# Kernel optimization log

Hardware: AMD Instinct MI355X
Metric: run time of the kernel (lower is better)

## Reference

```python
import jax, jax.numpy as jnp
import numpy as np
import math

N_HEAD = 16
ROPE_BASE = 10000.0

def _rope_cos_sin(seq_len, head_dim, dtype):
    inv_freq = 1.0 / (ROPE_BASE ** (jnp.arange(0, head_dim, 2, dtype=jnp.float32) / head_dim))
    t = jnp.arange(seq_len, dtype=jnp.float32)
    freqs = t[:, None] * inv_freq[None, :]            # [S, D/2]
    emb = jnp.concatenate([freqs, freqs], axis=-1)     # [S, D]
    # broadcast shape [1, 1, S, D] to match q/k [B, H, S, D]
    return jnp.cos(emb)[None, None].astype(dtype), jnp.sin(emb)[None, None].astype(dtype)

def _rotate_half(x):
    x1, x2 = jnp.split(x, 2, axis=-1)
    return jnp.concatenate([-x2, x1], axis=-1)

def setup_inputs() -> dict:
    key = jax.random.key(0)
    ks = jax.random.split(key, 5)
    B, S, E = 2, 2048, 1024
    x = jax.random.normal(ks[0], (B, S, E), dtype=jnp.float32)
    init = 1.0 / math.sqrt(E)
    Wq = jax.random.normal(ks[1], (E, E), dtype=jnp.float32) * init
    Wk = jax.random.normal(ks[2], (E, E), dtype=jnp.float32) * init
    Wv = jax.random.normal(ks[3], (E, E), dtype=jnp.float32) * init
    Wo = jax.random.normal(ks[4], (E, E), dtype=jnp.float32) * init
    # causal mask: True = masked (masked_fill with -inf)
    attn_mask = jnp.triu(jnp.ones((S, S), dtype=bool), k=1)
    return {"x": x, "Wq": Wq, "Wk": Wk, "Wv": Wv, "Wo": Wo, "attn_mask": attn_mask}

def reference(x, Wq, Wk, Wv, Wo, attn_mask):
    B, S, E = x.shape
    H = N_HEAD
    D = E // H
    # projections (torch Linear: y = x @ W.T), split heads -> [B, H, S, D]
    def proj(W):
        return jnp.einsum('bse,fe->bsf', x, W).reshape(B, S, H, D).transpose(0, 2, 1, 3)
    q, k, v = proj(Wq), proj(Wk), proj(Wv)
    cos, sin = _rope_cos_sin(S, D, x.dtype)
    q = q * cos + _rotate_half(q) * sin
    k = k * cos + _rotate_half(k) * sin
    scale = 1.0 / math.sqrt(D)
    scores = jnp.einsum('bhqd,bhkd->bhqk', q, k) * scale  # [B, H, S, S]
    scores = jnp.where(attn_mask[None, None], -jnp.inf, scores)
    attn = jax.nn.softmax(scores, axis=-1)
    out = jnp.einsum('bhqk,bhkd->bhqd', attn, v)           # [B, H, S, D]
    out = out.transpose(0, 2, 1, 3).reshape(B, S, E)
    return jnp.einsum('bse,fe->bsf', out, Wo)
```

## Files before the change

### kernel.cpp

```cpp
#include <hip/hip_runtime.h>
#include <hip/hip_bf16.h>

#define NB 2
#define NH 16
#define SEQ 2048
#define HD 64
#define EMB 1024

typedef unsigned short u16;
typedef unsigned int u32;
typedef __attribute__((ext_vector_type(8))) short bf16x8;
typedef __attribute__((ext_vector_type(4))) float f32x4;
typedef __attribute__((ext_vector_type(8))) unsigned short us8;

__device__ __forceinline__ float b2f(u16 u) {
    union { unsigned int i; float f; } v; v.i = ((unsigned int)u) << 16; return v.f;
}
__device__ __forceinline__ u16 f2b(float f) {
    union { float f; unsigned int i; } v; v.f = f;
    unsigned int x = v.i;
    return (u16)((x + 0x7FFFu + ((x >> 16) & 1u)) >> 16);
}
__device__ __forceinline__ u32 pk2(float a, float b) {
    union { __hip_bfloat162 h; u32 u; } v;
    v.h = __float22bfloat162_rn(make_float2(a, b));
    return v.u;
}

__device__ __forceinline__ void gld16(const u16* g, u16* l) {
    __builtin_amdgcn_global_load_lds((const __attribute__((address_space(1))) void*)g,
                                     (__attribute__((address_space(3))) void*)l, 16, 0, 0);
}

__global__ __launch_bounds__(256)
void detect_dtype_54571854463007(const u16* __restrict__ x, int* __restrict__ flag) {
    __shared__ int cnt;
    if (threadIdx.x == 0) cnt = 0;
    __syncthreads();
    const u16 v = x[threadIdx.x];
    const int e = (v >> 7) & 0xFF;
    if (e >= 110 && e <= 135) atomicAdd(&cnt, 1);
    __syncthreads();
    if (threadIdx.x == 0) *flag = (cnt >= 200) ? 1 : 0;
}

__device__ __forceinline__ void conv8(const void* src, u16* dst, int i, int isbf16) {
    if (isbf16) {
        *reinterpret_cast<uint4*>(dst + i) =
            *reinterpret_cast<const uint4*>((const u16*)src + i);
    } else {
        const float* s = (const float*)src + i;
        float4 a = *reinterpret_cast<const float4*>(s);
        float4 b = *reinterpret_cast<const float4*>(s + 4);
        us8 v;
        v[0] = f2b(a.x); v[1] = f2b(a.y); v[2] = f2b(a.z); v[3] = f2b(a.w);
        v[4] = f2b(b.x); v[5] = f2b(b.y); v[6] = f2b(b.z); v[7] = f2b(b.w);
        *reinterpret_cast<us8*>(dst + i) = v;
    }
}

__global__ __launch_bounds__(256)
void convert_54571854463007(const void* __restrict__ src, u16* __restrict__ dst,
                            const int* __restrict__ flagp, int n) {
    const int i = (blockIdx.x * 256 + threadIdx.x) * 8;
    if (i >= n) return;
    conv8(src, dst, i, *flagp);
}

__global__ __launch_bounds__(256)
void convertw_54571854463007(const void* __restrict__ w0, const void* __restrict__ w1,
                             const void* __restrict__ w2, const void* __restrict__ w3,
                             u16* __restrict__ dqkv, u16* __restrict__ dob,
                             const int* __restrict__ flagp) {
    const int NW = EMB * EMB;
    const int seg = blockIdx.y;
    const void* src = (seg == 0) ? w0 : (seg == 1) ? w1 : (seg == 2) ? w2 : w3;
    u16* dst = (seg < 3) ? (dqkv + (size_t)seg * NW) : dob;
    const int i = (blockIdx.x * 256 + threadIdx.x) * 8;
    conv8(src, dst, i, *flagp);
}

template<int OUT_MODE>
__global__ __launch_bounds__(256)
void gemm_mfma_54571854463007(const u16* __restrict__ A, const u16* __restrict__ Bw,
                              void* __restrict__ C, const int* __restrict__ flagp,
                              int M, int N, int K) {
    __shared__ __align__(16) u16 As[128 * 32];
    __shared__ __align__(16) u16 Bs[128 * 32];
    const int tid  = threadIdx.x;
    const int wave = tid >> 6, lane = tid & 63;
    const int quad = lane >> 4, fr = lane & 15;
    const int wr = (wave >> 1) * 64, wc = (wave & 1) * 64;
    const int m0 = blockIdx.y * 128, n0 = blockIdx.x * 128;
    const int r0 = tid >> 2;
    const int kc = (tid & 3) * 8;
    const f32x4 zz = {0.f, 0.f, 0.f, 0.f};
    f32x4 acc[4][4];
#pragma unroll
    for (int i = 0; i < 4; ++i)
#pragma unroll
        for (int j = 0; j < 4; ++j) acc[i][j] = zz;

    for (int k0 = 0; k0 < K; k0 += 32) {
        gld16(A  + (size_t)(m0 + r0) * K + k0 + kc,      &As[wave * 512]);
        gld16(A  + (size_t)(m0 + 64 + r0) * K + k0 + kc, &As[2048 + wave * 512]);
        gld16(Bw + (size_t)(n0 + r0) * K + k0 + kc,      &Bs[wave * 512]);
        gld16(Bw + (size_t)(n0 + 64 + r0) * K + k0 + kc, &Bs[2048 + wave * 512]);
        __syncthreads();
        bf16x8 af[4], bfr[4];
#pragma unroll
        for (int mi = 0; mi < 4; ++mi)
            af[mi] = *reinterpret_cast<const bf16x8*>(&As[(wr + mi * 16 + fr) * 32 + quad * 8]);
#pragma unroll
        for (int ni = 0; ni < 4; ++ni)
            bfr[ni] = *reinterpret_cast<const bf16x8*>(&Bs[(wc + ni * 16 + fr) * 32 + quad * 8]);
#pragma unroll
        for (int mi = 0; mi < 4; ++mi)
#pragma unroll
            for (int ni = 0; ni < 4; ++ni)
                acc[mi][ni] = __builtin_amdgcn_mfma_f32_16x16x32_bf16(af[mi], bfr[ni], acc[mi][ni], 0, 0, 0);
        __syncthreads();
    }

    if (OUT_MODE == 1) {
        const int t0 = n0 >> 10;
        if (t0 == 0) {
            const float SCL = 0.18033688011112042f;
#pragma unroll
            for (int mi = 0; mi < 4; ++mi)
#pragma unroll
                for (int ni = 0; ni < 4; ++ni)
#pragma unroll
                    for (int r = 0; r < 4; ++r) acc[mi][ni][r] *= SCL;
        }
        if (t0 < 2) {
            const float inv0 = __powf(10000.f, -(float)fr / 32.f);
            const float inv1 = __powf(10000.f, -(float)(fr + 16) / 32.f);
#pragma unroll
            for (int mi = 0; mi < 4; ++mi)
#pragma unroll
                for (int r = 0; r < 4; ++r) {
                    const int s = (m0 + wr + mi * 16 + quad * 4 + r) & (SEQ - 1);
#pragma unroll
                    for (int nl = 0; nl < 2; ++nl) {
                        float sn, cs;
                        __sincosf((float)s * (nl ? inv1 : inv0), &sn, &cs);
                        const float lo = acc[mi][nl][r], hi = acc[mi][nl + 2][r];
                        acc[mi][nl][r]     = lo * cs - hi * sn;
                        acc[mi][nl + 2][r] = hi * cs + lo * sn;
                    }
                }
        }
    }

    const int isbf16 = (OUT_MODE == 0) ? *flagp : 0;
    const size_t TS = (size_t)NB * NH * SEQ * HD;
#pragma unroll
    for (int mi = 0; mi < 4; ++mi)
#pragma unroll
        for (int ni = 0; ni < 4; ++ni)
#pragma unroll
            for (int r = 0; r < 4; ++r) {
                const int m = m0 + wr + mi * 16 + quad * 4 + r;
                const int n = n0 + wc + ni * 16 + fr;
                const float v = acc[mi][ni][r];
                if (OUT_MODE == 1) {
                    const int t = n >> 10, idx = n & 1023;
                    const int h = idx >> 6, d = idx & 63;
                    const int b = m >> 11, s = m & (SEQ - 1);
                    ((u16*)C)[t * TS + ((((size_t)b * NH + h) * SEQ + s) << 6) + d] = f2b(v);
                } else {
                    if (isbf16) ((u16*)C)[(size_t)m * N + n] = f2b(v);
                    else        ((float*)C)[(size_t)m * N + n] = v;
                }
            }
}

__device__ __forceinline__ void loadK_54571854463007(const u16* Kt, int fr, int quad,
                                                     bf16x8* kc) {
#pragma unroll
    for (int nt = 0; nt < 4; ++nt) {
        const u16* kp = Kt + (size_t)(nt * 16 + fr) * HD + quad * 8;
        kc[2 * nt]     = *reinterpret_cast<const bf16x8*>(kp);
        kc[2 * nt + 1] = *reinterpret_cast<const bf16x8*>(kp + 32);
    }
}

__global__ __launch_bounds__(256)
void flash_54571854463007(const u16* __restrict__ Q, const u16* __restrict__ K,
                          const u16* __restrict__ V, u16* __restrict__ AO) {
    __shared__ __align__(16) u16 Vt[2 * 4608];
    __shared__ __align__(16) u16 Ps[4608];
    const int tid  = threadIdx.x;
    const int w    = tid >> 6, lane = tid & 63;
    const int quad = lane >> 4, fr = lane & 15;
    const int lin = blockIdx.x;
    const int xcd = lin & 7;
    const int p   = lin >> 3;
    const int qt  = 31 - (p >> 2);
    const int bh  = xcd * 4 + (p & 3);
    const int h = bh & 15, b = bh >> 4;
    const size_t base = ((size_t)b * NH + h) * SEQ * HD;
    const int k2   = (tid & 31) * 2;
    const int key0 = (k2 & 3) * 16 + (k2 >> 2);
    const int d8   = ((tid >> 5) & 7) * 8;
    const int total = qt + 1;

    const bf16x8 ones = {(short)0x3F80, (short)0x3F80, (short)0x3F80, (short)0x3F80,
                         (short)0x3F80, (short)0x3F80, (short)0x3F80, (short)0x3F80};

    const u16* qp = Q + base + (size_t)(qt * 64 + w * 16 + fr) * HD + quad * 8;
    const bf16x8 aq0 = *reinterpret_cast<const bf16x8*>(qp);
    const bf16x8 aq1 = *reinterpret_cast<const bf16x8*>(qp + 32);

    bf16x8 kc[8], kn[8];
    loadK_54571854463007(K + base, fr, quad, kc);
    us8 vc0, vc1, vn0, vn1;
    {
        const u16* vs = V + base + (size_t)key0 * HD + d8;
        vc0 = *reinterpret_cast<const us8*>(vs);
        vc1 = *reinterpret_cast<const us8*>(vs + 16 * HD);
    }

    const f32x4 zz = {0.f, 0.f, 0.f, 0.f};
    f32x4 lacc = zz;
    f32x4 oacc[4];
#pragma unroll
    for (int nt = 0; nt < 4; ++nt) oacc[nt] = zz;

    for (int j = 0; j < total; ++j) {
        const int buf   = j & 1;
        const int kt    = j;
        const int vbase = buf * 4608;
#pragma unroll
        for (int jj = 0; jj < 8; ++jj) {
            const u32 pk = ((u32)(u16)vc1[jj] << 16) | (u32)(u16)vc0[jj];
            *reinterpret_cast<u32*>(&Vt[vbase + (d8 + jj) * 72 + k2]) = pk;
        }
        __syncthreads();
        if (j + 1 < total) {
            const int nkt = j + 1;
            loadK_54571854463007(K + base + (size_t)nkt * 64 * HD, fr, quad, kn);
            const u16* vs = V + base + (size_t)(nkt * 64 + key0) * HD + d8;
            vn0 = *reinterpret_cast<const us8*>(vs);
            vn1 = *reinterpret_cast<const us8*>(vs + 16 * HD);
        }
        f32x4 sa[4];
#pragma unroll
        for (int nt = 0; nt < 4; ++nt) {
            sa[nt] = __builtin_amdgcn_mfma_f32_16x16x32_bf16(aq0, kc[2 * nt], zz, 0, 0, 0);
            sa[nt] = __builtin_amdgcn_mfma_f32_16x16x32_bf16(aq1, kc[2 * nt + 1], sa[nt], 0, 0, 0);
        }
        if (kt == qt) {
#pragma unroll
            for (int nt = 0; nt < 4; ++nt)
#pragma unroll
                for (int r = 0; r < 4; ++r)
                    if (nt * 16 + fr > w * 16 + quad * 4 + r) sa[nt][r] = -__builtin_inff();
        }
#pragma unroll
        for (int r = 0; r < 4; ++r) {
            const float p0 = exp2f(sa[0][r]);
            const float p1 = exp2f(sa[1][r]);
            const float p2 = exp2f(sa[2][r]);
            const float p3 = exp2f(sa[3][r]);
            *reinterpret_cast<uint2*>(&Ps[(w * 16 + quad * 4 + r) * 72 + 4 * fr]) =
                make_uint2(pk2(p0, p1), pk2(p2, p3));
        }
        bf16x8 ap0 = *reinterpret_cast<const bf16x8*>(&Ps[(w * 16 + fr) * 72 + quad * 8]);
        bf16x8 ap1 = *reinterpret_cast<const bf16x8*>(&Ps[(w * 16 + fr) * 72 + 32 + quad * 8]);
        lacc = __builtin_amdgcn_mfma_f32_16x16x32_bf16(ap0, ones, lacc, 0, 0, 0);
        lacc = __builtin_amdgcn_mfma_f32_16x16x32_bf16(ap1, ones, lacc, 0, 0, 0);
#pragma unroll
        for (int nt = 0; nt < 4; ++nt) {
            bf16x8 bv0 = *reinterpret_cast<const bf16x8*>(&Vt[vbase + (nt * 16 + fr) * 72 + quad * 8]);
            bf16x8 bv1 = *reinterpret_cast<const bf16x8*>(&Vt[vbase + (nt * 16 + fr) * 72 + 32 + quad * 8]);
            oacc[nt] = __builtin_amdgcn_mfma_f32_16x16x32_bf16(ap0, bv0, oacc[nt], 0, 0, 0);
            oacc[nt] = __builtin_amdgcn_mfma_f32_16x16x32_bf16(ap1, bv1, oacc[nt], 0, 0, 0);
        }
#pragma unroll
        for (int i = 0; i < 8; ++i) kc[i] = kn[i];
        vc0 = vn0; vc1 = vn1;
    }
#pragma unroll
    for (int r = 0; r < 4; ++r) {
        const float inv = 1.0f / lacc[r];
        const int q = qt * 64 + w * 16 + quad * 4 + r;
#pragma unroll
        for (int nt = 0; nt < 4; ++nt)
            AO[(((size_t)b * SEQ + q) * NH + h) * HD + nt * 16 + fr] = f2b(oacc[nt][r] * inv);
    }
}

extern "C" void kernel_launch(void* const* d_in, const int* in_sizes, int n_in,
                              void* d_out, int out_size, void* d_ws, size_t ws_size,
                              hipStream_t stream) {
    (void)in_sizes; (void)n_in; (void)out_size; (void)ws_size;
    const void* x  = d_in[0];
    const void* Wq = d_in[1];
    const void* Wk = d_in[2];
    const void* Wv = d_in[3];
    const void* Wo = d_in[4];

    char* ws = (char*)d_ws;
    const size_t MB = 1024 * 1024;
    int* flag = (int*)ws;
    u16* xb   = (u16*)(ws + 64);
    u16* Wqkv = (u16*)(ws + 64 + 8 * MB);
    u16* Wob  = (u16*)(ws + 64 + 14 * MB);
    u16* Qb   = (u16*)(ws + 64 + 16 * MB);
    u16* Kb   = (u16*)(ws + 64 + 24 * MB);
    u16* Vb   = (u16*)(ws + 64 + 32 * MB);
    u16* AO   = xb;

    detect_dtype_54571854463007<<<1, 256, 0, stream>>>((const u16*)x, flag);

    const int NX = NB * SEQ * EMB;
    const int NW = EMB * EMB;
    convert_54571854463007<<<NX / 2048, 256, 0, stream>>>(x, xb, flag, NX);
    convertw_54571854463007<<<dim3(NW / 2048, 4), 256, 0, stream>>>(Wq, Wk, Wv, Wo, Wqkv, Wob, flag);

    const int M = NB * SEQ;
    gemm_mfma_54571854463007<1><<<dim3(3 * EMB / 128, M / 128), 256, 0, stream>>>(
        xb, Wqkv, Qb, flag, M, 3 * EMB, EMB);

    flash_54571854463007<<<dim3(1024), 256, 0, stream>>>(Qb, Kb, Vb, AO);

    gemm_mfma_54571854463007<0><<<dim3(EMB / 128, M / 128), 256, 0, stream>>>(
        AO, Wob, d_out, flag, M, EMB, EMB);
}
```

Before: 245.5 us.

## Stage K tiles in swizzled LDS and pass P through bpermute instead of LDS

K tiles now go through a double-buffered, XOR-swizzled LDS buffer using direct global-to-LDS loads (gld16) rather than per-lane register prefetch. The QK^T MFMA operands are swapped so scores come out transposed. This lets the softmax probabilities be redistributed across lanes with ds_bpermute instead of a round trip through the shared Ps buffer. Launch bounds request four blocks per CU to raise occupancy. The aim is to cut register pressure and LDS traffic, at the cost of more cross-lane permutes and a bigger LDS footprint for K.

Measured after the change: 214.4 us. 12.7% less time.

```diff
diff --git a/kernel.cpp b/kernel.cpp
--- a/kernel.cpp
+++ b/kernel.cpp
@@ -176,21 +176,11 @@
             }
 }
 
-__device__ __forceinline__ void loadK_54571854463007(const u16* Kt, int fr, int quad,
-                                                     bf16x8* kc) {
-#pragma unroll
-    for (int nt = 0; nt < 4; ++nt) {
-        const u16* kp = Kt + (size_t)(nt * 16 + fr) * HD + quad * 8;
-        kc[2 * nt]     = *reinterpret_cast<const bf16x8*>(kp);
-        kc[2 * nt + 1] = *reinterpret_cast<const bf16x8*>(kp + 32);
-    }
-}
-
-__global__ __launch_bounds__(256)
+__global__ __launch_bounds__(256, 4)
 void flash_54571854463007(const u16* __restrict__ Q, const u16* __restrict__ K,
                           const u16* __restrict__ V, u16* __restrict__ AO) {
+    __shared__ __align__(16) u16 Kt[2 * 4096];
     __shared__ __align__(16) u16 Vt[2 * 4608];
-    __shared__ __align__(16) u16 Ps[4608];
     const int tid  = threadIdx.x;
     const int w    = tid >> 6, lane = tid & 63;
     const int quad = lane >> 4, fr = lane & 15;
@@ -206,6 +196,15 @@
     const int d8   = ((tid >> 5) & 7) * 8;
     const int total = qt + 1;
 
+    const int krs = lane >> 3;
+    const int kch = ((lane & 7) ^ krs) * 8;
+    const int swz = fr & 7;
+    const int co0 = (quad ^ swz) * 8;
+    const int co1 = ((quad + 4) ^ swz) * 8;
+    const int bpA = ((quad >> 1) * 16 + fr) * 4;
+    const int bpB = bpA + 128;
+    const bool qo = (quad & 1) != 0;
+
     const bf16x8 ones = {(short)0x3F80, (short)0x3F80, (short)0x3F80, (short)0x3F80,
                          (short)0x3F80, (short)0x3F80, (short)0x3F80, (short)0x3F80};
 
@@ -213,8 +212,11 @@
     const bf16x8 aq0 = *reinterpret_cast<const bf16x8*>(qp);
     const bf16x8 aq1 = *reinterpret_cast<const bf16x8*>(qp + 32);
 
-    bf16x8 kc[8], kn[8];
-    loadK_54571854463007(K + base, fr, quad, kc);
+    {
+        const u16* Kg = K + base;
+        gld16(Kg + (size_t)((w * 2 + 0) * 8 + krs) * HD + kch, &Kt[(w * 2 + 0) * 512]);
+        gld16(Kg + (size_t)((w * 2 + 1) * 8 + krs) * HD + kch, &Kt[(w * 2 + 1) * 512]);
+    }
     us8 vc0, vc1, vn0, vn1;
     {
         const u16* vs = V + base + (size_t)key0 * HD + d8;
@@ -229,57 +231,74 @@
     for (int nt = 0; nt < 4; ++nt) oacc[nt] = zz;
 
     for (int j = 0; j < total; ++j) {
-        const int buf   = j & 1;
-        const int kt    = j;
-        const int vbase = buf * 4608;
+        const int buf = j & 1;
+        const int vb  = buf * 4608;
+        const int kb  = buf * 4096;
 #pragma unroll
         for (int jj = 0; jj < 8; ++jj) {
             const u32 pk = ((u32)(u16)vc1[jj] << 16) | (u32)(u16)vc0[jj];
-            *reinterpret_cast<u32*>(&Vt[vbase + (d8 + jj) * 72 + k2]) = pk;
+            *reinterpret_cast<u32*>(&Vt[vb + (d8 + jj) * 72 + k2]) = pk;
         }
         __syncthreads();
         if (j + 1 < total) {
-            const int nkt = j + 1;
-            loadK_54571854463007(K + base + (size_t)nkt * 64 * HD, fr, quad, kn);
-            const u16* vs = V + base + (size_t)(nkt * 64 + key0) * HD + d8;
+            const u16* Kg = K + base + (size_t)(j + 1) * 64 * HD;
+            const int kb1 = (buf ^ 1) * 4096;
+            gld16(Kg + (size_t)((w * 2 + 0) * 8 + krs) * HD + kch, &Kt[kb1 + (w * 2 + 0) * 512]);
+            gld16(Kg + (size_t)((w * 2 + 1) * 8 + krs) * HD + kch, &Kt[kb1 + (w * 2 + 1) * 512]);
+            const u16* vs = V + base + (size_t)((j + 1) * 64 + key0) * HD + d8;
             vn0 = *reinterpret_cast<const us8*>(vs);
             vn1 = *reinterpret_cast<const us8*>(vs + 16 * HD);
         }
         f32x4 sa[4];
 #pragma unroll
         for (int nt = 0; nt < 4; ++nt) {
-            sa[nt] = __builtin_amdgcn_mfma_f32_16x16x32_bf16(aq0, kc[2 * nt], zz, 0, 0, 0);
-            sa[nt] = __builtin_amdgcn_mfma_f32_16x16x32_bf16(aq1, kc[2 * nt + 1], sa[nt], 0, 0, 0);
-        }
-        if (kt == qt) {
+            const int rb = kb + (nt * 16 + fr) * 64;
+            const bf16x8 ka0 = *reinterpret_cast<const bf16x8*>(&Kt[rb + co0]);
+            const bf16x8 ka1 = *reinterpret_cast<const bf16x8*>(&Kt[rb + co1]);
+            sa[nt] = __builtin_amdgcn_mfma_f32_16x16x32_bf16(ka0, aq0, zz, 0, 0, 0);
+            sa[nt] = __builtin_amdgcn_mfma_f32_16x16x32_bf16(ka1, aq1, sa[nt], 0, 0, 0);
+        }
+        if (j == qt) {
 #pragma unroll
             for (int nt = 0; nt < 4; ++nt)
 #pragma unroll
                 for (int r = 0; r < 4; ++r)
-                    if (nt * 16 + fr > w * 16 + quad * 4 + r) sa[nt][r] = -__builtin_inff();
-        }
+                    if (nt * 16 + quad * 4 + r > w * 16 + fr) sa[nt][r] = -__builtin_inff();
+        }
+        u32 c01[4], c23[4];
 #pragma unroll
         for (int r = 0; r < 4; ++r) {
-            const float p0 = exp2f(sa[0][r]);
-            const float p1 = exp2f(sa[1][r]);
-            const float p2 = exp2f(sa[2][r]);
-            const float p3 = exp2f(sa[3][r]);
-            *reinterpret_cast<uint2*>(&Ps[(w * 16 + quad * 4 + r) * 72 + 4 * fr]) =
-                make_uint2(pk2(p0, p1), pk2(p2, p3));
-        }
-        bf16x8 ap0 = *reinterpret_cast<const bf16x8*>(&Ps[(w * 16 + fr) * 72 + quad * 8]);
-        bf16x8 ap1 = *reinterpret_cast<const bf16x8*>(&Ps[(w * 16 + fr) * 72 + 32 + quad * 8]);
-        lacc = __builtin_amdgcn_mfma_f32_16x16x32_bf16(ap0, ones, lacc, 0, 0, 0);
-        lacc = __builtin_amdgcn_mfma_f32_16x16x32_bf16(ap1, ones, lacc, 0, 0, 0);
+            c01[r] = pk2(exp2f(sa[0][r]), exp2f(sa[1][r]));
+            c23[r] = pk2(exp2f(sa[2][r]), exp2f(sa[3][r]));
+        }
+        u32 A01[4], A23[4], B01[4], B23[4];
+#pragma unroll
+        for (int r = 0; r < 4; ++r) {
+            A01[r] = (u32)__builtin_amdgcn_ds_bpermute(bpA, (int)c01[r]);
+            A23[r] = (u32)__builtin_amdgcn_ds_bpermute(bpA, (int)c23[r]);
+            B01[r] = (u32)__builtin_amdgcn_ds_bpermute(bpB, (int)c01[r]);
+            B23[r] = (u32)__builtin_amdgcn_ds_bpermute(bpB, (int)c23[r]);
+        }
+        union { u32 u[4]; bf16x8 v; } P0, P1;
+        P0.u[0] = qo ? A01[2] : A01[0];
+        P0.u[1] = qo ? A23[2] : A23[0];
+        P0.u[2] = qo ? A01[3] : A01[1];
+        P0.u[3] = qo ? A23[3] : A23[1];
+        P1.u[0] = qo ? B01[2] : B01[0];
+        P1.u[1] = qo ? B23[2] : B23[0];
+        P1.u[2] = qo ? B01[3] : B01[1];
+        P1.u[3] = qo ? B23[3] : B23[1];
+        const bf16x8 pa0 = P0.v;
+        const bf16x8 pa1 = P1.v;
+        lacc = __builtin_amdgcn_mfma_f32_16x16x32_bf16(pa0, ones, lacc, 0, 0, 0);
+        lacc = __builtin_amdgcn_mfma_f32_16x16x32_bf16(pa1, ones, lacc, 0, 0, 0);
 #pragma unroll
         for (int nt = 0; nt < 4; ++nt) {
-            bf16x8 bv0 = *reinterpret_cast<const bf16x8*>(&Vt[vbase + (nt * 16 + fr) * 72 + quad * 8]);
-            bf16x8 bv1 = *reinterpret_cast<const bf16x8*>(&Vt[vbase + (nt * 16 + fr) * 72 + 32 + quad * 8]);
-            oacc[nt] = __builtin_amdgcn_mfma_f32_16x16x32_bf16(ap0, bv0, oacc[nt], 0, 0, 0);
-            oacc[nt] = __builtin_amdgcn_mfma_f32_16x16x32_bf16(ap1, bv1, oacc[nt], 0, 0, 0);
-        }
-#pragma unroll
-        for (int i = 0; i < 8; ++i) kc[i] = kn[i];
+            const bf16x8 bv0 = *reinterpret_cast<const bf16x8*>(&Vt[vb + (nt * 16 + fr) * 72 + quad * 8]);
+            const bf16x8 bv1 = *reinterpret_cast<const bf16x8*>(&Vt[vb + (nt * 16 + fr) * 72 + 32 + quad * 8]);
+            oacc[nt] = __builtin_amdgcn_mfma_f32_16x16x32_bf16(pa0, bv0, oacc[nt], 0, 0, 0);
+            oacc[nt] = __builtin_amdgcn_mfma_f32_16x16x32_bf16(pa1, bv1, oacc[nt], 0, 0, 0);
+        }
         vc0 = vn0; vc1 = vn1;
     }
 #pragma unroll
```
